# Kernel tuning notes

Measured on AMD Instinct MI355X. Metric: run time of the kernel, lower is better.

The kernel has to match this reference:

```python
import jax, jax.numpy as jnp
import numpy as np

DIMS = 4

def mlp(x, W1, b1, W2, b2, W3, b3, Wo, bo):
    # x: (4,) -> scalar log(g_rr)
    h = jnp.tanh(x @ W1 + b1)
    h = jnp.tanh(h @ W2 + b2)
    h = jnp.tanh(h @ W3 + b3)
    return (h @ Wo + bo)[0]

def metric(x, params):
    # build_g: spherical metric with learned g_rr = exp(net(x))
    g_rr = jnp.exp(mlp(x, *params))
    r, th = x[1], x[2]
    diag = jnp.stack([-jnp.ones(()), g_rr, r ** 2, (r * jnp.sin(th)) ** 2])
    return jnp.diag(diag)  # (4,4)

def christoffel(x, params):
    g = metric(x, params)
    dg = jax.jacfwd(lambda xx: metric(xx, params))(x)  # dg[i,j,k] = d g_ij / d x^k
    g_inv = jnp.linalg.inv(g)
    # Gamma^a_bc = 0.5 g^{ad} (d_c g_db + d_b g_dc - d_d g_bc)
    sym = dg + jnp.transpose(dg, (0, 2, 1)) - jnp.transpose(dg, (2, 0, 1))
    gamma = 0.5 * jnp.einsum('ad,dbc->abc', g_inv, sym)
    return gamma, g_inv

def einstein_per_sample(x, params):
    gamma, g_inv = christoffel(x, params)
    # D[a,i,j,k] = d_k Gamma^a_ij (second nested forward-mode jacobian)
    D = jax.jacfwd(lambda xx: christoffel(xx, params)[0])(x)
    # R^a_bcd = d_c Gamma^a_db - d_d Gamma^a_cb + G^a_ce G^e_db - G^a_de G^e_cb
    riemann = (jnp.einsum('adbc->abcd', D) - jnp.einsum('acbd->abcd', D)
               + jnp.einsum('ace,edb->abcd', gamma, gamma)
               - jnp.einsum('ade,ecb->abcd', gamma, gamma))
    ricci = jnp.einsum('abad->bd', riemann)
    ricci_scalar = jnp.einsum('bd,bd->', g_inv, ricci)
    ricci_up = jnp.einsum('ac,bd,cd->ab', g_inv, g_inv, ricci)
    return ricci_up - 0.5 * g_inv * ricci_scalar  # contravariant Einstein tensor


def setup_inputs() -> dict:
    key = jax.random.key(0)
    ks = jax.random.split(key, 5)
    B, H = 8192, 256
    # coords in a well-conditioned region (avoid r ~ 0 which makes g singular)
    coords = jax.random.uniform(ks[0], (B, DIMS), dtype=jnp.float32) * 0.9 + 0.1
    def w(k, shape):
        fan_in = shape[0]
        return jax.random.normal(k, shape, dtype=jnp.float32) / np.sqrt(fan_in)
    return {
        'coords': coords,
        'W1': w(ks[1], (DIMS, H)), 'b1': jnp.zeros((H,), jnp.float32),
        'W2': w(ks[2], (H, H)),   'b2': jnp.zeros((H,), jnp.float32),
        'W3': w(ks[3], (H, H)),   'b3': jnp.zeros((H,), jnp.float32),
        'Wo': w(ks[4], (H, 1)),   'bo': jnp.zeros((1,), jnp.float32),
    }


def reference(coords, W1, b1, W2, b2, W3, b3, Wo, bo):
    params = (W1, b1, W2, b2, W3, b3, Wo, bo)
    # Batched Einstein tensor G^{ab}(x) for every sample: (B, 4, 4)
    return jax.vmap(lambda x: einstein_per_sample(x, params))(coords)
```

## Files before the change

### kernel.cpp

```cpp
#include <hip/hip_runtime.h>
#include <math.h>

typedef _Float16 half8 __attribute__((ext_vector_type(8)));
typedef float floatx4 __attribute__((ext_vector_type(4)));

#define HDIM 256
#define NC 15
#define NCP 16
#define SPB 8
#define GPT 2
#define MR 128
#define NWAVE 4
#define NT 4


__device__ __forceinline__ float ftanh(float x) {
    float e = __expf(2.f * x);
    return fmaf(-2.f, __builtin_amdgcn_rcpf(e + 1.f), 1.f);
}

__device__ __forceinline__ void einstein_tail(
    float f, const float* Gf, const float* Hs, float r, float th,
    float* __restrict__ outp)
{
    float Hf[4][4];
    {
        int qq = 0;
#pragma unroll
        for (int k = 0; k < 4; ++k)
#pragma unroll
            for (int l = k; l < 4; ++l) { Hf[k][l] = Hs[qq]; Hf[l][k] = Hs[qq]; ++qq; }
    }
    float sn = sinf(th), cs = cosf(th);
    float E  = expf(f);

    float gd[4] = {-1.f, E, r * r, r * r * sn * sn};
    float gi[4];
#pragma unroll
    for (int a = 0; a < 4; ++a) gi[a] = 1.f / gd[a];

    float dgv[4][4];
    float ddg[4][4][4];
#pragma unroll
    for (int a = 0; a < 4; ++a)
#pragma unroll
        for (int k = 0; k < 4; ++k) {
            dgv[a][k] = 0.f;
#pragma unroll
            for (int l = 0; l < 4; ++l) ddg[a][k][l] = 0.f;
        }
#pragma unroll
    for (int k = 0; k < 4; ++k) dgv[1][k] = E * Gf[k];
    dgv[2][1] = 2.f * r;
    dgv[3][1] = 2.f * r * sn * sn;
    dgv[3][2] = 2.f * r * r * sn * cs;
#pragma unroll
    for (int k = 0; k < 4; ++k)
#pragma unroll
        for (int l = 0; l < 4; ++l)
            ddg[1][k][l] = E * fmaf(Gf[k], Gf[l], Hf[k][l]);
    ddg[2][1][1] = 2.f;
    ddg[3][1][1] = 2.f * sn * sn;
    ddg[3][1][2] = 4.f * r * sn * cs;
    ddg[3][2][1] = 4.f * r * sn * cs;
    ddg[3][2][2] = 2.f * r * r * (cs * cs - sn * sn);

    auto SYMF = [&](int a, int i, int jx) -> float {
        float sy = 0.f;
        if (a == i)  sy += dgv[a][jx];
        if (a == jx) sy += dgv[a][i];
        if (i == jx) sy -= dgv[i][a];
        return sy;
    };
    auto DF = [&](int a, int i, int jx, int k) -> float {
        float ds = 0.f;
        if (a == i)  ds += ddg[a][jx][k];
        if (a == jx) ds += ddg[a][i][k];
        if (i == jx) ds -= ddg[i][a][k];
        return 0.5f * (gi[a] * ds - gi[a] * gi[a] * dgv[a][k] * SYMF(a, i, jx));
    };

    float Gm[4][4][4];
#pragma unroll
    for (int a = 0; a < 4; ++a)
#pragma unroll
        for (int i = 0; i < 4; ++i)
#pragma unroll
            for (int jx = 0; jx < 4; ++jx)
                Gm[a][i][jx] = 0.5f * gi[a] * SYMF(a, i, jx);

    float ric[4][4];
#pragma unroll
    for (int b = 0; b < 4; ++b)
#pragma unroll
        for (int d = 0; d < 4; ++d) {
            float sum = 0.f;
#pragma unroll
            for (int a = 0; a < 4; ++a) {
                sum += DF(a, d, b, a) - DF(a, a, b, d);
#pragma unroll
                for (int e = 0; e < 4; ++e)
                    sum += Gm[a][a][e] * Gm[e][d][b] - Gm[a][d][e] * Gm[e][a][b];
            }
            ric[b][d] = sum;
        }

    float Rs = 0.f;
#pragma unroll
    for (int b = 0; b < 4; ++b) Rs += gi[b] * ric[b][b];

#pragma unroll
    for (int a = 0; a < 4; ++a)
#pragma unroll
        for (int b = 0; b < 4; ++b) {
            float v = gi[a] * gi[b] * ric[a][b];
            if (a == b) v -= 0.5f * gi[a] * Rs;
            outp[a * 4 + b] = v;
        }
}

__global__ __launch_bounds__(64) void einstein_k(
    const float* __restrict__ coords, const float* __restrict__ bo,
    float* io, int B)
{
    const int s = blockIdx.x * 64 + threadIdx.x;
    if (s >= B) return;
    float4 f0 = *(const float4*)&io[s * 16 + 0];
    float4 f1 = *(const float4*)&io[s * 16 + 4];
    float4 f2 = *(const float4*)&io[s * 16 + 8];
    float4 f3 = *(const float4*)&io[s * 16 + 12];
    float f = f0.x + bo[0];
    float Gf[4] = {f0.y, f0.z, f0.w, f1.x};
    float Hs[10] = {f1.y, f1.z, f1.w, f2.x, f2.y, f2.z, f2.w, f3.x, f3.y, f3.z};
    float r  = coords[s * 4 + 1];
    float th = coords[s * 4 + 2];
    float res[16];
    einstein_tail(f, Gf, Hs, r, th, res);
#pragma unroll
    for (int e = 0; e < 4; ++e)
        *(float4*)&io[s * 16 + e * 4] =
            make_float4(res[e*4+0], res[e*4+1], res[e*4+2], res[e*4+3]);
}

__global__ __launch_bounds__(256) void pack_wt(
    const float* __restrict__ W2, const float* __restrict__ W3,
    _Float16* __restrict__ Wt)
{
    __shared__ float t[64][65];
    const int m    = blockIdx.x >> 4;
    const float* W = m ? W3 : W2;
    const int tile = blockIdx.x & 15;
    const int k0 = (tile >> 2) * 64, j0 = (tile & 3) * 64;
    const int tx = threadIdx.x & 63, ty = threadIdx.x >> 6;
#pragma unroll
    for (int i = 0; i < 16; ++i) {
        int k = ty + i * 4;
        t[k][tx] = W[(k0 + k) * HDIM + j0 + tx];
    }
    __syncthreads();
#pragma unroll
    for (int i = 0; i < 16; ++i) {
        int jj = ty + i * 4;
        Wt[(size_t)m * HDIM * HDIM + (j0 + jj) * HDIM + k0 + tx] =
            (_Float16)t[tx][jj];
    }
}

template <bool TW>
__global__ __launch_bounds__(512, 2) void mlp_fused(
    const float* __restrict__ coords,
    const float* __restrict__ W1, const float* __restrict__ b1,
    const float* __restrict__ W2, const float* __restrict__ b2,
    const float* __restrict__ W3, const float* __restrict__ b3,
    const float* __restrict__ Wo,
    const _Float16* __restrict__ Wt,
    float* __restrict__ out, int B)
{
    __shared__ __align__(16) _Float16 st[2][MR * HDIM];
    __shared__ float part[2][GPT][NWAVE][SPB][NCP];

    const int tid  = threadIdx.x;
    const int team = tid >> 8;
    const int ttid = tid & 255;
    const int w    = ttid >> 6;
    const int lane = tid & 63;
    const int col  = lane & 15;
    const int q    = lane >> 4;
    const int s0   = blockIdx.x * (2 * GPT * SPB);

    _Float16* __restrict__ stT = st[team];

    floatx4 acc[8][NT];

    auto f4get = [](const float4& v, int i) -> float {
        switch (i & 3) { case 0: return v.x; case 1: return v.y;
                         case 2: return v.z; default: return v.w; }
    };

    auto sbase = [&](int g) { return s0 + (team * GPT + g) * SPB; };

    auto produce1 = [&](int g) {
        const int sl = ttid & 7;
        const int tc = ttid >> 3;
        int ss = sbase(g) + sl; if (ss >= B) ss = B - 1;
        const float x0 = coords[ss * 4 + 0];
        const float x1 = coords[ss * 4 + 1];
        const float x2 = coords[ss * 4 + 2];
        const float x3 = coords[ss * 4 + 3];
        const int jg = tc * 8;
        float4 wa[4][2];
#pragma unroll
        for (int k = 0; k < 4; ++k) {
            wa[k][0] = *(const float4*)&W1[k * HDIM + jg];
            wa[k][1] = *(const float4*)&W1[k * HDIM + jg + 4];
        }
        float4 bb0 = *(const float4*)&b1[jg];
        float4 bb1 = *(const float4*)&b1[jg + 4];
        half8 ch[NC];
#pragma unroll
        for (int jj = 0; jj < 8; ++jj) {
            const int h = jj >> 2;
            float w0 = f4get(wa[0][h], jj), w1 = f4get(wa[1][h], jj);
            float w2v = f4get(wa[2][h], jj), w3v = f4get(wa[3][h], jj);
            float a = f4get(h ? bb1 : bb0, jj);
            a = fmaf(x0, w0, a); a = fmaf(x1, w1, a);
            a = fmaf(x2, w2v, a); a = fmaf(x3, w3v, a);
            float v = ftanh(a), tp = 1.f - v * v, m2 = -2.f * v * tp;
            float g4[4] = {w0, w1, w2v, w3v};
            ch[0][jj] = (_Float16)v;
#pragma unroll
            for (int k = 0; k < 4; ++k) ch[1 + k][jj] = (_Float16)(tp * g4[k]);
            int idx = 5;
#pragma unroll
            for (int aa = 0; aa < 4; ++aa)
#pragma unroll
                for (int bb2 = aa; bb2 < 4; ++bb2) {
                    ch[idx][jj] = (_Float16)(m2 * g4[aa] * g4[bb2]); ++idx;
                }
        }
#pragma unroll
        for (int c = 0; c < NC; ++c) {
            const int m = 16 * (c >> 1) + 4 * (sl >> 1) + 2 * (sl & 1) + (c & 1);
            const int addr = m * HDIM + (((tc ^ m) & 31) << 3);
            *(half8*)&stT[addr] = ch[c];
        }
    };

    auto gemm_full = [&](const float* __restrict__ W, int layer) {
        half8 bf[2][NT];
#pragma unroll
        for (int nt = 0; nt < NT; ++nt) {
            const int j = w * 64 + nt * 16 + col;
            if constexpr (TW) {
                bf[0][nt] = *(const half8*)&Wt[((size_t)layer * HDIM + j) * HDIM + q * 8];
            } else {
#pragma unroll
                for (int i = 0; i < 8; ++i)
                    bf[0][nt][i] = (_Float16)W[(q * 8 + i) * HDIM + j];
            }
        }
        const floatx4 z = {0.f, 0.f, 0.f, 0.f};
#pragma unroll
        for (int ks = 0; ks < 8; ++ks) {
            const int cur = ks & 1, nxt = cur ^ 1;
            if (ks < 7) {
                const int kg2 = (ks + 1) * 32 + q * 8;
#pragma unroll
                for (int nt = 0; nt < NT; ++nt) {
                    const int j = w * 64 + nt * 16 + col;
                    if constexpr (TW) {
                        bf[nxt][nt] = *(const half8*)&Wt[((size_t)layer * HDIM + j) * HDIM + kg2];
                    } else {
#pragma unroll
                        for (int i = 0; i < 8; ++i)
                            bf[nxt][nt][i] = (_Float16)W[(kg2 + i) * HDIM + j];
                    }
                }
            }
            const int lc = ks * 4 + q;
            __builtin_amdgcn_s_setprio(1);
            half8 af[8];
#pragma unroll
            for (int mt = 0; mt < 8; ++mt) {
                const int m = 16 * mt + col;
                af[mt] = *(const half8*)&stT[m * HDIM + (((lc ^ m) & 31) << 3)];
            }
#pragma unroll
            for (int mt = 0; mt < 8; ++mt)
#pragma unroll
                for (int nt = 0; nt < NT; ++nt)
                    acc[mt][nt] = __builtin_amdgcn_mfma_f32_16x16x32_f16(
                        af[mt], bf[cur][nt], (ks == 0) ? z : acc[mt][nt], 0, 0, 0);
            __builtin_amdgcn_s_setprio(0);
        }
    };

    auto transform_store = [&](const float* __restrict__ b) {
#pragma unroll
        for (int nt = 0; nt < NT; ++nt) {
            const int j = w * 64 + nt * 16 + col;
            const int jc = j >> 3, jb = j & 7;
            const float bj = b[j];
#pragma unroll
            for (int sv = 0; sv < 2; ++sv) {
                float pre[NCP];
#pragma unroll
                for (int c = 0; c < NCP; ++c)
                    pre[c] = acc[c >> 1][nt][sv * 2 + (c & 1)];
                pre[0] += bj;
                float v = ftanh(pre[0]), tp = 1.f - v * v, m2 = -2.f * v * tp;
                float g4[4] = {pre[1], pre[2], pre[3], pre[4]};
                float ns[NC];
                ns[0] = v;
#pragma unroll
                for (int k = 0; k < 4; ++k) ns[1 + k] = tp * g4[k];
                int idx = 5;
#pragma unroll
                for (int aa = 0; aa < 4; ++aa)
#pragma unroll
                    for (int bb2 = aa; bb2 < 4; ++bb2) {
                        ns[idx] = fmaf(tp, pre[idx], m2 * g4[aa] * g4[bb2]); ++idx;
                    }
#pragma unroll
                for (int c = 0; c < NC; ++c) {
                    const int m = 16 * (c >> 1) + 4 * q + 2 * sv + (c & 1);
                    stT[m * HDIM + (((jc ^ m) & 31) << 3) + jb] = (_Float16)ns[c];
                }
            }
        }
    };

    auto epilogue_part = [&](int g, const float* __restrict__ b) {
        float wo[NT];
#pragma unroll
        for (int nt = 0; nt < NT; ++nt) wo[nt] = Wo[w * 64 + nt * 16 + col];

        float on2[2][NC];
#pragma unroll
        for (int sv = 0; sv < 2; ++sv)
#pragma unroll
            for (int c = 0; c < NC; ++c) on2[sv][c] = 0.f;
#pragma unroll
        for (int nt = 0; nt < NT; ++nt) {
            const float bj = b[w * 64 + nt * 16 + col];
#pragma unroll
            for (int sv = 0; sv < 2; ++sv) {
                float pre[NCP];
#pragma unroll
                for (int c = 0; c < NCP; ++c)
                    pre[c] = acc[c >> 1][nt][sv * 2 + (c & 1)];
                pre[0] += bj;
                float v = ftanh(pre[0]), tp = 1.f - v * v, m2 = -2.f * v * tp;
                float g4[4] = {pre[1], pre[2], pre[3], pre[4]};
                on2[sv][0] = fmaf(wo[nt], v, on2[sv][0]);
#pragma unroll
                for (int k = 0; k < 4; ++k)
                    on2[sv][1 + k] = fmaf(wo[nt], tp * g4[k], on2[sv][1 + k]);
                int idx = 5;
#pragma unroll
                for (int aa = 0; aa < 4; ++aa)
#pragma unroll
                    for (int bb2 = aa; bb2 < 4; ++bb2) {
                        on2[sv][idx] = fmaf(wo[nt],
                            fmaf(tp, pre[idx], m2 * g4[aa] * g4[bb2]), on2[sv][idx]);
                        ++idx;
                    }
            }
        }
#pragma unroll
        for (int mask = 1; mask < 16; mask <<= 1)
#pragma unroll
            for (int sv = 0; sv < 2; ++sv)
#pragma unroll
                for (int c = 0; c < NC; ++c)
                    on2[sv][c] += __shfl_xor(on2[sv][c], mask, 64);
        if (col == 0) {
#pragma unroll
            for (int sv = 0; sv < 2; ++sv)
#pragma unroll
                for (int c = 0; c < NC; ++c)
                    part[team][g][w][2 * q + sv][c] = on2[sv][c];
        }
    };

    auto final_reduce = [&]() {
        if (ttid < SPB * NC) {
            const int sl = ttid / NC, c = ttid % NC;
#pragma unroll
            for (int g = 0; g < GPT; ++g) {
                float v = 0.f;
#pragma unroll
                for (int ww = 0; ww < NWAVE; ++ww)
                    v += part[team][g][ww][sl][c];
                int s = sbase(g) + sl;
                if (s < B) out[s * 16 + c] = v;
            }
        }
    };

    if (team == 0) produce1(0);
    __syncthreads();
    if (team == 0) gemm_full(W2, 0);
    else produce1(0);
    __syncthreads();
    if (team == 0) transform_store(b2);
    else gemm_full(W2, 0);
    __syncthreads();
    if (team == 0) gemm_full(W3, 1);
    else transform_store(b2);
    __syncthreads();
    if (team == 0) { epilogue_part(0, b3); produce1(1); }
    else gemm_full(W3, 1);
    __syncthreads();
    if (team == 0) gemm_full(W2, 0);
    else { epilogue_part(0, b3); produce1(1); }
    __syncthreads();
    if (team == 0) transform_store(b2);
    else gemm_full(W2, 0);
    __syncthreads();
    if (team == 0) gemm_full(W3, 1);
    else transform_store(b2);
    __syncthreads();
    if (team == 0) epilogue_part(1, b3);
    else gemm_full(W3, 1);
    __syncthreads();
    if (team == 0) final_reduce();
    else epilogue_part(1, b3);
    __syncthreads();
    if (team == 1) final_reduce();
}

extern "C" void kernel_launch(void* const* d_in, const int* in_sizes, int n_in,
                              void* d_out, int out_size, void* d_ws, size_t ws_size,
                              hipStream_t stream) {
    const float* coords = (const float*)d_in[0];
    const float* W1 = (const float*)d_in[1];
    const float* b1 = (const float*)d_in[2];
    const float* W2 = (const float*)d_in[3];
    const float* b2 = (const float*)d_in[4];
    const float* W3 = (const float*)d_in[5];
    const float* b3 = (const float*)d_in[6];
    const float* Wo = (const float*)d_in[7];
    const float* bo = (const float*)d_in[8];
    float* out = (float*)d_out;
    const int B = in_sizes[0] / 4;
    const int spb_blk = 2 * GPT * SPB;
    const int nblocks = (B + spb_blk - 1) / spb_blk;

    const size_t wt_bytes = (size_t)2 * HDIM * HDIM * sizeof(_Float16);
    if (ws_size >= wt_bytes) {
        _Float16* Wt = (_Float16*)d_ws;
        pack_wt<<<32, 256, 0, stream>>>(W2, W3, Wt);
        mlp_fused<true><<<nblocks, 512, 0, stream>>>(
            coords, W1, b1, W2, b2, W3, b3, Wo, Wt, out, B);
    } else {
        mlp_fused<false><<<nblocks, 512, 0, stream>>>(
            coords, W1, b1, W2, b2, W3, b3, Wo, nullptr, out, B);
    }
    einstein_k<<<(B + 63) / 64, 64, 0, stream>>>(coords, bo, out, B);
}
```

Measured before the change: 116.1 us.

## Switch MLP GEMMs from 16x16x32 to 32x32x16 MFMA tiles

Replaces the 16x16x32 f16 MFMA tiling (8x4 tiles per wave) with 32x32x16 MFMA (4x2 tiles), and remaps the LDS row layout so each sample's 16 jet components land in one 32-row accumulator column group. This cuts the number of LDS A-fragment loads and B-fragment loads per FLOP and lets each lane hold all 16 components of a sample, at the cost of twice as many k-steps and a longer shuffle reduction (5 steps instead of 4) in the epilogue.

Measured after the change: 130.1 us. +12.1%, slower.

```diff
diff --git a/kernel.cpp b/kernel.cpp
--- a/kernel.cpp
+++ b/kernel.cpp
@@ -2,7 +2,7 @@
 #include <math.h>
 
 typedef _Float16 half8 __attribute__((ext_vector_type(8)));
-typedef float floatx4 __attribute__((ext_vector_type(4)));
+typedef float floatx16 __attribute__((ext_vector_type(16)));
 
 #define HDIM 256
 #define NC 15
@@ -11,7 +11,8 @@
 #define GPT 2
 #define MR 128
 #define NWAVE 4
-#define NT 4
+#define NMT 4
+#define NNT 2
 
 
 __device__ __forceinline__ float ftanh(float x) {
@@ -184,13 +185,13 @@
     const int ttid = tid & 255;
     const int w    = ttid >> 6;
     const int lane = tid & 63;
-    const int col  = lane & 15;
-    const int q    = lane >> 4;
+    const int co   = lane & 31;
+    const int hi   = lane >> 5;
     const int s0   = blockIdx.x * (2 * GPT * SPB);
 
     _Float16* __restrict__ stT = st[team];
 
-    floatx4 acc[8][NT];
+    floatx16 acc[NMT][NNT];
 
     auto f4get = [](const float4& v, int i) -> float {
         switch (i & 3) { case 0: return v.x; case 1: return v.y;
@@ -198,6 +199,10 @@
     };
 
     auto sbase = [&](int g) { return s0 + (team * GPT + g) * SPB; };
+
+    auto mrow = [](int sl, int c) {
+        return 32 * (sl >> 1) + 4 * (sl & 1) + (c & 3) + 8 * (c >> 2);
+    };
 
     auto produce1 = [&](int g) {
         const int sl = ttid & 7;
@@ -240,34 +245,36 @@
         }
 #pragma unroll
         for (int c = 0; c < NC; ++c) {
-            const int m = 16 * (c >> 1) + 4 * (sl >> 1) + 2 * (sl & 1) + (c & 1);
+            const int m = mrow(sl, c);
             const int addr = m * HDIM + (((tc ^ m) & 31) << 3);
             *(half8*)&stT[addr] = ch[c];
         }
     };
 
     auto gemm_full = [&](const float* __restrict__ W, int layer) {
-        half8 bf[2][NT];
-#pragma unroll
-        for (int nt = 0; nt < NT; ++nt) {
-            const int j = w * 64 + nt * 16 + col;
+        half8 bf[2][NNT];
+#pragma unroll
+        for (int nt = 0; nt < NNT; ++nt) {
+            const int j = w * 64 + nt * 32 + co;
+            const int kg = hi * 8;
             if constexpr (TW) {
-                bf[0][nt] = *(const half8*)&Wt[((size_t)layer * HDIM + j) * HDIM + q * 8];
+                bf[0][nt] = *(const half8*)&Wt[((size_t)layer * HDIM + j) * HDIM + kg];
             } else {
 #pragma unroll
                 for (int i = 0; i < 8; ++i)
-                    bf[0][nt][i] = (_Float16)W[(q * 8 + i) * HDIM + j];
-            }
-        }
-        const floatx4 z = {0.f, 0.f, 0.f, 0.f};
-#pragma unroll
-        for (int ks = 0; ks < 8; ++ks) {
+                    bf[0][nt][i] = (_Float16)W[(kg + i) * HDIM + j];
+            }
+        }
+        const floatx16 z = {0.f,0.f,0.f,0.f,0.f,0.f,0.f,0.f,
+                            0.f,0.f,0.f,0.f,0.f,0.f,0.f,0.f};
+#pragma unroll
+        for (int ks = 0; ks < 16; ++ks) {
             const int cur = ks & 1, nxt = cur ^ 1;
-            if (ks < 7) {
-                const int kg2 = (ks + 1) * 32 + q * 8;
-#pragma unroll
-                for (int nt = 0; nt < NT; ++nt) {
-                    const int j = w * 64 + nt * 16 + col;
+            if (ks < 15) {
+                const int kg2 = (ks + 1) * 16 + hi * 8;
+#pragma unroll
+                for (int nt = 0; nt < NNT; ++nt) {
+                    const int j = w * 64 + nt * 32 + co;
                     if constexpr (TW) {
                         bf[nxt][nt] = *(const half8*)&Wt[((size_t)layer * HDIM + j) * HDIM + kg2];
                     } else {
@@ -277,19 +284,19 @@
                     }
                 }
             }
-            const int lc = ks * 4 + q;
+            const int lchunk = ks * 2 + hi;
             __builtin_amdgcn_s_setprio(1);
-            half8 af[8];
-#pragma unroll
-            for (int mt = 0; mt < 8; ++mt) {
-                const int m = 16 * mt + col;
-                af[mt] = *(const half8*)&stT[m * HDIM + (((lc ^ m) & 31) << 3)];
-            }
-#pragma unroll
-            for (int mt = 0; mt < 8; ++mt)
-#pragma unroll
-                for (int nt = 0; nt < NT; ++nt)
-                    acc[mt][nt] = __builtin_amdgcn_mfma_f32_16x16x32_f16(
+            half8 af[NMT];
+#pragma unroll
+            for (int mt = 0; mt < NMT; ++mt) {
+                const int m = 32 * mt + co;
+                af[mt] = *(const half8*)&stT[m * HDIM + (((lchunk ^ m) & 31) << 3)];
+            }
+#pragma unroll
+            for (int mt = 0; mt < NMT; ++mt)
+#pragma unroll
+                for (int nt = 0; nt < NNT; ++nt)
+                    acc[mt][nt] = __builtin_amdgcn_mfma_f32_32x32x16_f16(
                         af[mt], bf[cur][nt], (ks == 0) ? z : acc[mt][nt], 0, 0, 0);
             __builtin_amdgcn_s_setprio(0);
         }
@@ -297,16 +304,16 @@
 
     auto transform_store = [&](const float* __restrict__ b) {
 #pragma unroll
-        for (int nt = 0; nt < NT; ++nt) {
-            const int j = w * 64 + nt * 16 + col;
+        for (int nt = 0; nt < NNT; ++nt) {
+            const int j = w * 64 + nt * 32 + co;
             const int jc = j >> 3, jb = j & 7;
             const float bj = b[j];
 #pragma unroll
-            for (int sv = 0; sv < 2; ++sv) {
+            for (int mt = 0; mt < NMT; ++mt) {
+                const int sl = 2 * mt + hi;
                 float pre[NCP];
 #pragma unroll
-                for (int c = 0; c < NCP; ++c)
-                    pre[c] = acc[c >> 1][nt][sv * 2 + (c & 1)];
+                for (int c = 0; c < NCP; ++c) pre[c] = acc[mt][nt][c];
                 pre[0] += bj;
                 float v = ftanh(pre[0]), tp = 1.f - v * v, m2 = -2.f * v * tp;
                 float g4[4] = {pre[1], pre[2], pre[3], pre[4]};
@@ -323,7 +330,7 @@
                     }
 #pragma unroll
                 for (int c = 0; c < NC; ++c) {
-                    const int m = 16 * (c >> 1) + 4 * q + 2 * sv + (c & 1);
+                    const int m = mrow(sl, c);
                     stT[m * HDIM + (((jc ^ m) & 31) << 3) + jb] = (_Float16)ns[c];
                 }
             }
@@ -331,55 +338,52 @@
     };
 
     auto epilogue_part = [&](int g, const float* __restrict__ b) {
-        float wo[NT];
-#pragma unroll
-        for (int nt = 0; nt < NT; ++nt) wo[nt] = Wo[w * 64 + nt * 16 + col];
-
-        float on2[2][NC];
-#pragma unroll
-        for (int sv = 0; sv < 2; ++sv)
-#pragma unroll
-            for (int c = 0; c < NC; ++c) on2[sv][c] = 0.f;
-#pragma unroll
-        for (int nt = 0; nt < NT; ++nt) {
-            const float bj = b[w * 64 + nt * 16 + col];
-#pragma unroll
-            for (int sv = 0; sv < 2; ++sv) {
+        float on[NMT][NC];
+#pragma unroll
+        for (int mt = 0; mt < NMT; ++mt)
+#pragma unroll
+            for (int c = 0; c < NC; ++c) on[mt][c] = 0.f;
+#pragma unroll
+        for (int nt = 0; nt < NNT; ++nt) {
+            const int j = w * 64 + nt * 32 + co;
+            const float wo = Wo[j];
+            const float bj = b[j];
+#pragma unroll
+            for (int mt = 0; mt < NMT; ++mt) {
                 float pre[NCP];
 #pragma unroll
-                for (int c = 0; c < NCP; ++c)
-                    pre[c] = acc[c >> 1][nt][sv * 2 + (c & 1)];
+                for (int c = 0; c < NCP; ++c) pre[c] = acc[mt][nt][c];
                 pre[0] += bj;
                 float v = ftanh(pre[0]), tp = 1.f - v * v, m2 = -2.f * v * tp;
                 float g4[4] = {pre[1], pre[2], pre[3], pre[4]};
-                on2[sv][0] = fmaf(wo[nt], v, on2[sv][0]);
+                on[mt][0] = fmaf(wo, v, on[mt][0]);
 #pragma unroll
                 for (int k = 0; k < 4; ++k)
-                    on2[sv][1 + k] = fmaf(wo[nt], tp * g4[k], on2[sv][1 + k]);
+                    on[mt][1 + k] = fmaf(wo, tp * g4[k], on[mt][1 + k]);
                 int idx = 5;
 #pragma unroll
                 for (int aa = 0; aa < 4; ++aa)
 #pragma unroll
                     for (int bb2 = aa; bb2 < 4; ++bb2) {
-                        on2[sv][idx] = fmaf(wo[nt],
-                            fmaf(tp, pre[idx], m2 * g4[aa] * g4[bb2]), on2[sv][idx]);
+                        on[mt][idx] = fmaf(wo,
+                            fmaf(tp, pre[idx], m2 * g4[aa] * g4[bb2]), on[mt][idx]);
                         ++idx;
                     }
             }
         }
 #pragma unroll
-        for (int mask = 1; mask < 16; mask <<= 1)
-#pragma unroll
-            for (int sv = 0; sv < 2; ++sv)
+        for (int mask = 1; mask < 32; mask <<= 1)
+#pragma unroll
+            for (int mt = 0; mt < NMT; ++mt)
 #pragma unroll
                 for (int c = 0; c < NC; ++c)
-                    on2[sv][c] += __shfl_xor(on2[sv][c], mask, 64);
-        if (col == 0) {
-#pragma unroll
-            for (int sv = 0; sv < 2; ++sv)
+                    on[mt][c] += __shfl_xor(on[mt][c], mask, 64);
+        if (co == 0) {
+#pragma unroll
+            for (int mt = 0; mt < NMT; ++mt)
 #pragma unroll
                 for (int c = 0; c < NC; ++c)
-                    part[team][g][w][2 * q + sv][c] = on2[sv][c];
+                    part[team][g][w][2 * mt + hi][c] = on[mt][c];
         }
     };
 
```
